# Optimization experiments

Measured on AMD Instinct MI355X. Metric: run time of the kernel, lower is better.

The kernel has to match this reference:

```python
import jax, jax.numpy as jnp
import numpy as np

B, T, D = 4, 4096, 2048
W_SCALE = 0.02


def setup_inputs() -> dict:
    key = jax.random.key(0)
    ks = jax.random.split(key, 10)
    x = jax.random.normal(ks[0], (B, T, D), dtype=jnp.float32)
    Wk = jax.random.normal(ks[1], (D, D), dtype=jnp.float32) * W_SCALE
    Wv = jax.random.normal(ks[2], (D, D), dtype=jnp.float32) * W_SCALE
    Wr = jax.random.normal(ks[3], (D, D), dtype=jnp.float32) * W_SCALE
    Wo = jax.random.normal(ks[4], (D, D), dtype=jnp.float32) * W_SCALE
    bk = jnp.zeros((D,), jnp.float32)
    bv = jnp.zeros((D,), jnp.float32)
    br = jnp.zeros((D,), jnp.float32)
    bo = jnp.zeros((D,), jnp.float32)
    tmk = jax.random.uniform(ks[5], (D,), dtype=jnp.float32)
    tmv = jax.random.uniform(ks[6], (D,), dtype=jnp.float32)
    tmr = jax.random.uniform(ks[7], (D,), dtype=jnp.float32)
    u = jax.random.normal(ks[8], (D,), dtype=jnp.float32) * 0.1
    w = jax.random.uniform(ks[9], (D,), dtype=jnp.float32)  # positive decay
    return {"x": x, "Wk": Wk, "bk": bk, "Wv": Wv, "bv": bv, "Wr": Wr, "br": br,
            "Wo": Wo, "bo": bo, "tmk": tmk, "tmv": tmv, "tmr": tmr, "u": u, "w": w}


def reference(x, Wk, bk, Wv, bv, Wr, br, Wo, bo, tmk, tmv, tmr, u, w):
    # time-shift: xs[:, t] = x[:, t-1], xs[:, 0] = 0  (ZeroPad2d((0,0,1,-1)))
    xs = jnp.pad(x, ((0, 0), (1, 0), (0, 0)))[:, :-1]
    k = x * tmk + xs * (1.0 - tmk)
    v = x * tmv + xs * (1.0 - tmv)
    r = jax.nn.silu(x * tmr + xs * (1.0 - tmr))
    # torch nn.Linear: y = x @ W.T + b
    k = jnp.einsum('btd,ed->bte', k, Wk) + bk
    v = jnp.einsum('btd,ed->bte', v, Wv) + bv
    r = jnp.einsum('btd,ed->bte', r, Wr) + br

    def step(carry, kv_t):
        a, b = carry  # (B, D) each
        k_t, v_t = kv_t
        t = jnp.maximum(u + k_t, w)
        e1 = jnp.exp(-w - t)
        e2 = jnp.exp(u + k_t - t)
        a = e1 * a + e2 * v_t
        b = e1 * b + e2
        return (a, b), a / b

    a0 = jnp.zeros((x.shape[0], x.shape[2]), x.dtype)
    b0 = jnp.zeros_like(a0)
    # scan over time: (T, B, D)
    _, wkv = jax.lax.scan(step, (a0, b0), (k.transpose(1, 0, 2), v.transpose(1, 0, 2)))
    wkv = wkv.transpose(1, 0, 2)  # (B, T, D)
    return jnp.einsum('btd,ed->bte', wkv * r, Wo) + bo
```

## Files before the change

kernel.cpp:

```cpp
#include <hip/hip_runtime.h>
#include <hip/hip_bf16.h>

#define Bb 4
#define Tt 4096
#define Dd 2048
#define Mm (Bb*Tt)
#define CHUNK 64
#define NCHUNK (Tt/CHUNK)

typedef short  short8  __attribute__((ext_vector_type(8)));
typedef float  floatx4 __attribute__((ext_vector_type(4)));

static __device__ __forceinline__ short f2bf(float f) {
    union { float f; unsigned u; } x; x.f = f;
    unsigned r = x.u + 0x7fffu + ((x.u >> 16) & 1u);
    return (short)(r >> 16);
}
static __device__ __forceinline__ float bf2f(short s) {
    union { unsigned u; float f; } x; x.u = ((unsigned)(unsigned short)s) << 16;
    return x.f;
}
static __device__ __forceinline__ float siluf(float v) { return v / (1.f + __expf(-v)); }
static __device__ __forceinline__ float mixf(float xv, float sv, float tv) {
    return fmaf(tv, xv - sv, sv);
}

#define GLDS16(gp, lp) __builtin_amdgcn_global_load_lds( \
    (const __attribute__((address_space(1))) void*)(gp), \
    (__attribute__((address_space(3))) void*)(lp), 16, 0, 0)

static __device__ __forceinline__ short8 pack8(float4 a, float4 b) {
    short8 r;
    r[0]=f2bf(a.x); r[1]=f2bf(a.y); r[2]=f2bf(a.z); r[3]=f2bf(a.w);
    r[4]=f2bf(b.x); r[5]=f2bf(b.y); r[6]=f2bf(b.z); r[7]=f2bf(b.w);
    return r;
}

__global__ __launch_bounds__(256)
void prep_w(const float* __restrict__ w0, const float* __restrict__ w1,
            const float* __restrict__ w2, const float* __restrict__ w3,
            short* __restrict__ o0, short* __restrict__ o1,
            short* __restrict__ o2, short* __restrict__ o3)
{
    const float* s; short* d;
    switch (blockIdx.y) {
        case 0: s = w0; d = o0; break;
        case 1: s = w1; d = o1; break;
        case 2: s = w2; d = o2; break;
        default: s = w3; d = o3; break;
    }
    const size_t e = ((size_t)blockIdx.x * 256 + threadIdx.x) * 8;
    float4 a = *(const float4*)(s + e);
    float4 b = *(const float4*)(s + e + 4);
    *(short8*)(d + e) = pack8(a, b);
}

__global__ __launch_bounds__(256)
void prep_a(const float* __restrict__ x,
            const float* __restrict__ tmk, const float* __restrict__ tmv,
            const float* __restrict__ tmr,
            short* __restrict__ ka, short* __restrict__ va, short* __restrict__ ra)
{
    const size_t e = ((size_t)blockIdx.x * 256 + threadIdx.x) * 8;
    const size_t row = e >> 11;
    const int    col = (int)(e & (Dd - 1));
    const int    t   = (int)(row & (Tt - 1));

    const float* xp = x + e;
    float4 x0 = *(const float4*)xp, x1 = *(const float4*)(xp + 4);
    float4 s0 = make_float4(0,0,0,0), s1 = make_float4(0,0,0,0);
    if (t > 0) { s0 = *(const float4*)(xp - Dd); s1 = *(const float4*)(xp - Dd + 4); }

    float4 tk0 = *(const float4*)(tmk + col), tk1 = *(const float4*)(tmk + col + 4);
    float4 tv0 = *(const float4*)(tmv + col), tv1 = *(const float4*)(tmv + col + 4);
    float4 tr0 = *(const float4*)(tmr + col), tr1 = *(const float4*)(tmr + col + 4);

    float4 k0 = make_float4(mixf(x0.x,s0.x,tk0.x), mixf(x0.y,s0.y,tk0.y),
                            mixf(x0.z,s0.z,tk0.z), mixf(x0.w,s0.w,tk0.w));
    float4 k1 = make_float4(mixf(x1.x,s1.x,tk1.x), mixf(x1.y,s1.y,tk1.y),
                            mixf(x1.z,s1.z,tk1.z), mixf(x1.w,s1.w,tk1.w));
    float4 v0 = make_float4(mixf(x0.x,s0.x,tv0.x), mixf(x0.y,s0.y,tv0.y),
                            mixf(x0.z,s0.z,tv0.z), mixf(x0.w,s0.w,tv0.w));
    float4 v1 = make_float4(mixf(x1.x,s1.x,tv1.x), mixf(x1.y,s1.y,tv1.y),
                            mixf(x1.z,s1.z,tv1.z), mixf(x1.w,s1.w,tv1.w));
    float4 r0 = make_float4(siluf(mixf(x0.x,s0.x,tr0.x)), siluf(mixf(x0.y,s0.y,tr0.y)),
                            siluf(mixf(x0.z,s0.z,tr0.z)), siluf(mixf(x0.w,s0.w,tr0.w)));
    float4 r1 = make_float4(siluf(mixf(x1.x,s1.x,tr1.x)), siluf(mixf(x1.y,s1.y,tr1.y)),
                            siluf(mixf(x1.z,s1.z,tr1.z)), siluf(mixf(x1.w,s1.w,tr1.w)));

    *(short8*)(ka + e) = pack8(k0, k1);
    *(short8*)(va + e) = pack8(v0, v1);
    *(short8*)(ra + e) = pack8(r0, r1);
}

template<int OUTBF>
__global__ __launch_bounds__(256)
void gemm_bf16(const short* __restrict__ A, const short* __restrict__ B,
               const float* __restrict__ bias, void* __restrict__ Cout)
{
    __shared__ short As[128*32];
    __shared__ short Bs[128*32];

    const int tid  = threadIdx.x;
    const int lane = tid & 63, wave = tid >> 6;
    const int row0 = blockIdx.x * 128;
    const int col0 = blockIdx.y * 128;

    const int srow = wave * 32 + (lane >> 2);
    const int scol = (lane & 3) * 8;
    const short* Ag0 = A + (size_t)(row0 + srow) * Dd + scol;
    const short* Ag1 = Ag0 + (size_t)16 * Dd;
    const short* Bg0 = B + (size_t)(col0 + srow) * Dd + scol;
    const short* Bg1 = Bg0 + (size_t)16 * Dd;
    short* Al0 = As + (wave * 32     ) * 32;
    short* Al1 = As + (wave * 32 + 16) * 32;
    short* Bl0 = Bs + (wave * 32     ) * 32;
    short* Bl1 = Bs + (wave * 32 + 16) * 32;

    const int wm = (wave >> 1) * 64, wn = (wave & 1) * 64;
    const int fm = lane & 15, fq = lane >> 4;

    floatx4 acc[4][4];
    #pragma unroll
    for (int i = 0; i < 4; i++)
        #pragma unroll
        for (int j = 0; j < 4; j++) acc[i][j] = (floatx4){0.f,0.f,0.f,0.f};

    for (int k0 = 0; k0 < Dd; k0 += 32) {
        __syncthreads();
        GLDS16(Ag0, Al0);
        GLDS16(Ag1, Al1);
        GLDS16(Bg0, Bl0);
        GLDS16(Bg1, Bl1);
        Ag0 += 32; Ag1 += 32; Bg0 += 32; Bg1 += 32;
        __syncthreads();

        short8 af[4], bfv[4];
        #pragma unroll
        for (int i = 0; i < 4; i++)
            af[i] = *(const short8*)(As + (wm + i*16 + fm)*32 + fq*8);
        #pragma unroll
        for (int j = 0; j < 4; j++)
            bfv[j] = *(const short8*)(Bs + (wn + j*16 + fm)*32 + fq*8);
        #pragma unroll
        for (int i = 0; i < 4; i++)
            #pragma unroll
            for (int j = 0; j < 4; j++)
                acc[i][j] = __builtin_amdgcn_mfma_f32_16x16x32_bf16(af[i], bfv[j], acc[i][j], 0, 0, 0);
    }

    #pragma unroll
    for (int j = 0; j < 4; j++) {
        const int gc = col0 + wn + j*16 + fm;
        const float bj = bias[gc];
        #pragma unroll
        for (int i = 0; i < 4; i++) {
            const int gr = row0 + wm + i*16 + fq*4;
            #pragma unroll
            for (int r = 0; r < 4; r++) {
                const float v = acc[i][j][r] + bj;
                if constexpr (OUTBF)
                    ((short*)Cout)[(size_t)(gr + r) * Dd + gc] = f2bf(v);
                else
                    ((float*)Cout)[(size_t)(gr + r) * Dd + gc] = v;
            }
        }
    }
}

__global__ __launch_bounds__(256)
void scan1(const short* __restrict__ K, const short* __restrict__ V,
           const float* __restrict__ u, const float* __restrict__ w,
           float* __restrict__ Asum, float* __restrict__ Bsum, float* __restrict__ Dsum)
{
    const int c = blockIdx.x, b = blockIdx.y;
    const int d = blockIdx.z * 256 + threadIdx.x;
    const float uu = u[d], ww = w[d];
    const size_t base = ((size_t)(b*Tt + c*CHUNK)) * Dd + d;
    float a = 0.f, bb = 0.f, dd = 1.f;
    #pragma unroll 4
    for (int t = 0; t < CHUNK; t++) {
        const float k = bf2f(K[base + (size_t)t*Dd]);
        const float v = bf2f(V[base + (size_t)t*Dd]);
        const float tt = fmaxf(uu + k, ww);
        const float e1 = __expf(-ww - tt);
        const float e2 = __expf(uu + k - tt);
        a  = e1*a  + e2*v;
        bb = e1*bb + e2;
        dd *= e1;
    }
    const size_t idx = ((size_t)c*Bb + b) * Dd + d;
    Asum[idx] = a; Bsum[idx] = bb; Dsum[idx] = dd;
}

__global__ __launch_bounds__(256)
void scan2(const float* __restrict__ Asum, const float* __restrict__ Bsum,
           const float* __restrict__ Dsum, float* __restrict__ Sa, float* __restrict__ Sb)
{
    const int g = blockIdx.x * 256 + threadIdx.x;
    float a = 0.f, bb = 0.f;
    for (int c = 0; c < NCHUNK; c++) {
        const size_t idx = (size_t)c * (Bb*Dd) + g;
        Sa[idx] = a; Sb[idx] = bb;
        const float dd = Dsum[idx];
        a  = dd*a  + Asum[idx];
        bb = dd*bb + Bsum[idx];
    }
}

__global__ __launch_bounds__(256)
void scan3(const short* __restrict__ K, const short* __restrict__ V,
           const short* __restrict__ R,
           const float* __restrict__ Sa, const float* __restrict__ Sb,
           const float* __restrict__ u, const float* __restrict__ w,
           short* __restrict__ AF)
{
    const int c = blockIdx.x, b = blockIdx.y;
    const int d = blockIdx.z * 256 + threadIdx.x;
    const float uu = u[d], ww = w[d];
    const size_t sidx = ((size_t)c*Bb + b) * Dd + d;
    float a = Sa[sidx], bb = Sb[sidx];
    const size_t base = ((size_t)(b*Tt + c*CHUNK)) * Dd + d;
    #pragma unroll 4
    for (int t = 0; t < CHUNK; t++) {
        const float k = bf2f(K[base + (size_t)t*Dd]);
        const float v = bf2f(V[base + (size_t)t*Dd]);
        const float tt = fmaxf(uu + k, ww);
        const float e1 = __expf(-ww - tt);
        const float e2 = __expf(uu + k - tt);
        a  = e1*a  + e2*v;
        bb = e1*bb + e2;
        const float wkv = a / bb;
        const float r = bf2f(R[base + (size_t)t*Dd]);
        AF[base + (size_t)t*Dd] = f2bf(wkv * r);
    }
}

extern "C" void kernel_launch(void* const* d_in, const int* in_sizes, int n_in,
                              void* d_out, int out_size, void* d_ws, size_t ws_size,
                              hipStream_t stream)
{
    const float* x   = (const float*)d_in[0];
    const float* Wk  = (const float*)d_in[1];
    const float* bk  = (const float*)d_in[2];
    const float* Wv  = (const float*)d_in[3];
    const float* bv  = (const float*)d_in[4];
    const float* Wr  = (const float*)d_in[5];
    const float* br  = (const float*)d_in[6];
    const float* Wo  = (const float*)d_in[7];
    const float* bo  = (const float*)d_in[8];
    const float* tmk = (const float*)d_in[9];
    const float* tmv = (const float*)d_in[10];
    const float* tmr = (const float*)d_in[11];
    const float* u   = (const float*)d_in[12];
    const float* w   = (const float*)d_in[13];

    char* ws = (char*)d_ws;
    short* Wkb  = (short*)(ws + 0x00000000ull);
    short* Wvb  = (short*)(ws + 0x00800000ull);
    short* Wrb  = (short*)(ws + 0x01000000ull);
    short* Wob  = (short*)(ws + 0x01800000ull);
    short* ka   = (short*)(ws + 0x02000000ull);
    short* va   = (short*)(ws + 0x06000000ull);
    short* ra   = (short*)(ws + 0x0A000000ull);
    short* Kb   = (short*)(ws + 0x0E000000ull);
    short* Vb   = (short*)(ws + 0x12000000ull);
    short* Rb   = (short*)(ws + 0x16000000ull);
    float* Asum = (float*)(ws + 0x1A000000ull);
    float* Bsum = (float*)(ws + 0x1A200000ull);
    float* Dsum = (float*)(ws + 0x1A400000ull);
    float* Sa   = (float*)(ws + 0x1A600000ull);
    float* Sb   = (float*)(ws + 0x1A800000ull);
    short* AF   = ka;

    prep_w<<<dim3(2048, 4), 256, 0, stream>>>(Wk, Wv, Wr, Wo, Wkb, Wvb, Wrb, Wob);
    prep_a<<<dim3(16384), 256, 0, stream>>>(x, tmk, tmv, tmr, ka, va, ra);

    dim3 gg(Mm/128, Dd/128);
    gemm_bf16<1><<<gg, 256, 0, stream>>>(ka, Wkb, bk, Kb);
    gemm_bf16<1><<<gg, 256, 0, stream>>>(va, Wvb, bv, Vb);
    gemm_bf16<1><<<gg, 256, 0, stream>>>(ra, Wrb, br, Rb);

    scan1<<<dim3(NCHUNK, Bb, Dd/256), 256, 0, stream>>>(Kb, Vb, u, w, Asum, Bsum, Dsum);
    scan2<<<dim3((Bb*Dd)/256), 256, 0, stream>>>(Asum, Bsum, Dsum, Sa, Sb);
    scan3<<<dim3(NCHUNK, Bb, Dd/256), 256, 0, stream>>>(Kb, Vb, Rb, Sa, Sb, u, w, AF);

    gemm_bf16<0><<<gg, 256, 0, stream>>>(AF, Wob, bo, (float*)d_out);
}
```

Measured before the change: 1.142 ms.

## Use 256x256 pipelined GEMM tiles and vectorize chunked scan kernels

Replaces the 128x128 single-buffered GEMM with a 256x256-tile, 512-thread kernel. The new kernel uses a 4-stage LDS ring with direct global-to-LDS loads, XOR-swizzled LDS addressing, grouped block ordering for L2 reuse, and split barriers with priority bumps around the MFMA bursts. The aim is to cut global traffic per FLOP and hide load latency behind compute. The scan kernels now process 8 channels per thread with 16-byte vector loads and stores, which raises register use and lowers the number of scan blocks.

```diff
diff --git a/kernel.cpp b/kernel.cpp
--- a/kernel.cpp
+++ b/kernel.cpp
@@ -7,6 +7,7 @@
 #define Mm (Bb*Tt)
 #define CHUNK 64
 #define NCHUNK (Tt/CHUNK)
+#define NT (Dd/32)
 
 typedef short  short8  __attribute__((ext_vector_type(8)));
 typedef float  floatx4 __attribute__((ext_vector_type(4)));
@@ -28,6 +29,12 @@
 #define GLDS16(gp, lp) __builtin_amdgcn_global_load_lds( \
     (const __attribute__((address_space(1))) void*)(gp), \
     (__attribute__((address_space(3))) void*)(lp), 16, 0, 0)
+
+#define FENCE() asm volatile("" ::: "memory")
+#define BAR()   do { FENCE(); __builtin_amdgcn_s_barrier(); FENCE(); } while (0)
+#define WAIT_LGKM0() asm volatile("s_waitcnt lgkmcnt(0)" ::: "memory")
+#define WAIT_VM8()   asm volatile("s_waitcnt vmcnt(8)" ::: "memory")
+#define WAIT_VM0()   asm volatile("s_waitcnt vmcnt(0)" ::: "memory")
 
 static __device__ __forceinline__ short8 pack8(float4 a, float4 b) {
     short8 r;
@@ -94,67 +101,132 @@
 }
 
 template<int OUTBF>
-__global__ __launch_bounds__(256)
-void gemm_bf16(const short* __restrict__ A, const short* __restrict__ B,
-               const float* __restrict__ bias, void* __restrict__ Cout)
-{
-    __shared__ short As[128*32];
-    __shared__ short Bs[128*32];
+__global__ __launch_bounds__(512)
+void gemm256(const short* __restrict__ A, const short* __restrict__ B,
+             const float* __restrict__ bias, void* __restrict__ Cout)
+{
+    __shared__ short As[4*8192];
+    __shared__ short Bs[4*8192];
 
     const int tid  = threadIdx.x;
-    const int lane = tid & 63, wave = tid >> 6;
-    const int row0 = blockIdx.x * 128;
-    const int col0 = blockIdx.y * 128;
-
-    const int srow = wave * 32 + (lane >> 2);
-    const int scol = (lane & 3) * 8;
-    const short* Ag0 = A + (size_t)(row0 + srow) * Dd + scol;
-    const short* Ag1 = Ag0 + (size_t)16 * Dd;
-    const short* Bg0 = B + (size_t)(col0 + srow) * Dd + scol;
-    const short* Bg1 = Bg0 + (size_t)16 * Dd;
-    short* Al0 = As + (wave * 32     ) * 32;
-    short* Al1 = As + (wave * 32 + 16) * 32;
-    short* Bl0 = Bs + (wave * 32     ) * 32;
-    short* Bl1 = Bs + (wave * 32 + 16) * 32;
-
-    const int wm = (wave >> 1) * 64, wn = (wave & 1) * 64;
+    const int lane = tid & 63, wv = tid >> 6;
+
+    const int orig = blockIdx.x;
+    const int wg   = (orig & 7) * 64 + (orig >> 3);
+    const int row0 = (wg & 63) * 256;
+    const int col0 = (wg >> 6) * 256;
+
+    const int lofs  = (lane * 16) ^ ((lane >> 3) << 4);
+    const int lrow  = lofs >> 6;
+    const int lcol8 = (lofs >> 4) & 3;
+    const short* Ag = A + (size_t)(row0 + wv * 32 + lrow) * Dd + lcol8 * 8;
+    const short* Bg = B + (size_t)(col0 + wv * 32 + lrow) * Dd + lcol8 * 8;
+    short* Asw = As + wv * 1024;
+    short* Bsw = Bs + wv * 1024;
+
+#define STAGE_A(bufi) do { \
+    GLDS16(Ag,                 Asw + (bufi)*8192); \
+    GLDS16(Ag + (size_t)16*Dd, Asw + (bufi)*8192 + 512); \
+    Ag += 32; } while (0)
+#define STAGE_B(bufi) do { \
+    GLDS16(Bg,                 Bsw + (bufi)*8192); \
+    GLDS16(Bg + (size_t)16*Dd, Bsw + (bufi)*8192 + 512); \
+    Bg += 32; } while (0)
+
     const int fm = lane & 15, fq = lane >> 4;
-
-    floatx4 acc[4][4];
-    #pragma unroll
-    for (int i = 0; i < 4; i++)
+    const int wm = (wv >> 2) * 128;
+    const int wn = (wv & 3) * 64;
+    const int rA = wm + fm, rB = wn + fm;
+    const char* aP = (const char*)As + (((rA * 64) | (fq * 16)) ^ (((rA >> 1) & 7) << 4));
+    const char* bP = (const char*)Bs + (((rB * 64) | (fq * 16)) ^ (((rB >> 1) & 7) << 4));
+
+    floatx4 acc[8][4];
+    #pragma unroll
+    for (int i = 0; i < 8; i++)
         #pragma unroll
         for (int j = 0; j < 4; j++) acc[i][j] = (floatx4){0.f,0.f,0.f,0.f};
 
-    for (int k0 = 0; k0 < Dd; k0 += 32) {
-        __syncthreads();
-        GLDS16(Ag0, Al0);
-        GLDS16(Ag1, Al1);
-        GLDS16(Bg0, Bl0);
-        GLDS16(Bg1, Bl1);
-        Ag0 += 32; Ag1 += 32; Bg0 += 32; Bg1 += 32;
-        __syncthreads();
-
-        short8 af[4], bfv[4];
+    short8 a_[4], b_[4];
+
+    STAGE_A(0); STAGE_B(0);
+    STAGE_A(1); STAGE_B(1);
+    STAGE_A(2); STAGE_B(2);
+    WAIT_VM8();
+    BAR();
+
+    for (int t = 0; t < NT - 3; ++t) {
+        const int bi = t & 3, nb = (t + 3) & 3;
+        #pragma unroll
+        for (int j = 0; j < 4; j++) b_[j] = *(const short8*)(bP + bi * 16384 + j * 1024);
+        #pragma unroll
+        for (int i = 0; i < 4; i++) a_[i] = *(const short8*)(aP + bi * 16384 + i * 1024);
+        STAGE_A(nb);
+        BAR();
+        WAIT_LGKM0(); __builtin_amdgcn_sched_barrier(0);
+        __builtin_amdgcn_s_setprio(1);
         #pragma unroll
         for (int i = 0; i < 4; i++)
-            af[i] = *(const short8*)(As + (wm + i*16 + fm)*32 + fq*8);
-        #pragma unroll
-        for (int j = 0; j < 4; j++)
-            bfv[j] = *(const short8*)(Bs + (wn + j*16 + fm)*32 + fq*8);
+            #pragma unroll
+            for (int j = 0; j < 4; j++)
+                acc[i][j] = __builtin_amdgcn_mfma_f32_16x16x32_bf16(a_[i], b_[j], acc[i][j], 0, 0, 0);
+        __builtin_amdgcn_s_setprio(0);
+        BAR();
+        #pragma unroll
+        for (int i = 0; i < 4; i++) a_[i] = *(const short8*)(aP + bi * 16384 + (4 + i) * 1024);
+        STAGE_B(nb);
+        WAIT_VM8();
+        BAR();
+        WAIT_LGKM0(); __builtin_amdgcn_sched_barrier(0);
+        __builtin_amdgcn_s_setprio(1);
         #pragma unroll
         for (int i = 0; i < 4; i++)
             #pragma unroll
             for (int j = 0; j < 4; j++)
-                acc[i][j] = __builtin_amdgcn_mfma_f32_16x16x32_bf16(af[i], bfv[j], acc[i][j], 0, 0, 0);
-    }
+                acc[4+i][j] = __builtin_amdgcn_mfma_f32_16x16x32_bf16(a_[i], b_[j], acc[4+i][j], 0, 0, 0);
+        __builtin_amdgcn_s_setprio(0);
+        BAR();
+    }
+
+    WAIT_VM0();
+    BAR();
+    for (int t = NT - 3; t < NT; ++t) {
+        const int bi = t & 3;
+        #pragma unroll
+        for (int j = 0; j < 4; j++) b_[j] = *(const short8*)(bP + bi * 16384 + j * 1024);
+        #pragma unroll
+        for (int i = 0; i < 4; i++) a_[i] = *(const short8*)(aP + bi * 16384 + i * 1024);
+        BAR();
+        WAIT_LGKM0(); __builtin_amdgcn_sched_barrier(0);
+        __builtin_amdgcn_s_setprio(1);
+        #pragma unroll
+        for (int i = 0; i < 4; i++)
+            #pragma unroll
+            for (int j = 0; j < 4; j++)
+                acc[i][j] = __builtin_amdgcn_mfma_f32_16x16x32_bf16(a_[i], b_[j], acc[i][j], 0, 0, 0);
+        __builtin_amdgcn_s_setprio(0);
+        BAR();
+        #pragma unroll
+        for (int i = 0; i < 4; i++) a_[i] = *(const short8*)(aP + bi * 16384 + (4 + i) * 1024);
+        BAR();
+        WAIT_LGKM0(); __builtin_amdgcn_sched_barrier(0);
+        __builtin_amdgcn_s_setprio(1);
+        #pragma unroll
+        for (int i = 0; i < 4; i++)
+            #pragma unroll
+            for (int j = 0; j < 4; j++)
+                acc[4+i][j] = __builtin_amdgcn_mfma_f32_16x16x32_bf16(a_[i], b_[j], acc[4+i][j], 0, 0, 0);
+        __builtin_amdgcn_s_setprio(0);
+        BAR();
+    }
+#undef STAGE_A
+#undef STAGE_B
 
     #pragma unroll
     for (int j = 0; j < 4; j++) {
         const int gc = col0 + wn + j*16 + fm;
         const float bj = bias[gc];
         #pragma unroll
-        for (int i = 0; i < 4; i++) {
+        for (int i = 0; i < 8; i++) {
             const int gr = row0 + wm + i*16 + fq*4;
             #pragma unroll
             for (int r = 0; r < 4; r++) {
@@ -174,23 +246,29 @@
            float* __restrict__ Asum, float* __restrict__ Bsum, float* __restrict__ Dsum)
 {
     const int c = blockIdx.x, b = blockIdx.y;
-    const int d = blockIdx.z * 256 + threadIdx.x;
-    const float uu = u[d], ww = w[d];
-    const size_t base = ((size_t)(b*Tt + c*CHUNK)) * Dd + d;
-    float a = 0.f, bb = 0.f, dd = 1.f;
-    #pragma unroll 4
+    const int d0 = threadIdx.x * 8;
+    float uu[8], ww[8], a[8], bb[8], dd[8];
+    #pragma unroll
+    for (int e = 0; e < 8; e++) { uu[e]=u[d0+e]; ww[e]=w[d0+e]; a[e]=0.f; bb[e]=0.f; dd[e]=1.f; }
+    const size_t base = ((size_t)(b*Tt + c*CHUNK)) * Dd + d0;
+    #pragma unroll 2
     for (int t = 0; t < CHUNK; t++) {
-        const float k = bf2f(K[base + (size_t)t*Dd]);
-        const float v = bf2f(V[base + (size_t)t*Dd]);
-        const float tt = fmaxf(uu + k, ww);
-        const float e1 = __expf(-ww - tt);
-        const float e2 = __expf(uu + k - tt);
-        a  = e1*a  + e2*v;
-        bb = e1*bb + e2;
-        dd *= e1;
-    }
-    const size_t idx = ((size_t)c*Bb + b) * Dd + d;
-    Asum[idx] = a; Bsum[idx] = bb; Dsum[idx] = dd;
+        short8 kv = *(const short8*)(K + base + (size_t)t*Dd);
+        short8 vv = *(const short8*)(V + base + (size_t)t*Dd);
+        #pragma unroll
+        for (int e = 0; e < 8; e++) {
+            const float k = bf2f(kv[e]), v = bf2f(vv[e]);
+            const float tt = fmaxf(uu[e] + k, ww[e]);
+            const float e1 = __expf(-ww[e] - tt);
+            const float e2 = __expf(uu[e] + k - tt);
+            a[e]  = e1*a[e]  + e2*v;
+            bb[e] = e1*bb[e] + e2;
+            dd[e] *= e1;
+        }
+    }
+    const size_t idx = ((size_t)c*Bb + b) * Dd + d0;
+    #pragma unroll
+    for (int e = 0; e < 8; e++) { Asum[idx+e]=a[e]; Bsum[idx+e]=bb[e]; Dsum[idx+e]=dd[e]; }
 }
 
 __global__ __launch_bounds__(256)
@@ -216,23 +294,29 @@
            short* __restrict__ AF)
 {
     const int c = blockIdx.x, b = blockIdx.y;
-    const int d = blockIdx.z * 256 + threadIdx.x;
-    const float uu = u[d], ww = w[d];
-    const size_t sidx = ((size_t)c*Bb + b) * Dd + d;
-    float a = Sa[sidx], bb = Sb[sidx];
-    const size_t base = ((size_t)(b*Tt + c*CHUNK)) * Dd + d;
-    #pragma unroll 4
+    const int d0 = threadIdx.x * 8;
+    float uu[8], ww[8], a[8], bb[8];
+    const size_t sidx = ((size_t)c*Bb + b) * Dd + d0;
+    #pragma unroll
+    for (int e = 0; e < 8; e++) { uu[e]=u[d0+e]; ww[e]=w[d0+e]; a[e]=Sa[sidx+e]; bb[e]=Sb[sidx+e]; }
+    const size_t base = ((size_t)(b*Tt + c*CHUNK)) * Dd + d0;
+    #pragma unroll 2
     for (int t = 0; t < CHUNK; t++) {
-        const float k = bf2f(K[base + (size_t)t*Dd]);
-        const float v = bf2f(V[base + (size_t)t*Dd]);
-        const float tt = fmaxf(uu + k, ww);
-        const float e1 = __expf(-ww - tt);
-        const float e2 = __expf(uu + k - tt);
-        a  = e1*a  + e2*v;
-        bb = e1*bb + e2;
-        const float wkv = a / bb;
-        const float r = bf2f(R[base + (size_t)t*Dd]);
-        AF[base + (size_t)t*Dd] = f2bf(wkv * r);
+        short8 kv = *(const short8*)(K + base + (size_t)t*Dd);
+        short8 vv = *(const short8*)(V + base + (size_t)t*Dd);
+        short8 rv = *(const short8*)(R + base + (size_t)t*Dd);
+        short8 ov;
+        #pragma unroll
+        for (int e = 0; e < 8; e++) {
+            const float k = bf2f(kv[e]), v = bf2f(vv[e]);
+            const float tt = fmaxf(uu[e] + k, ww[e]);
+            const float e1 = __expf(-ww[e] - tt);
+            const float e2 = __expf(uu[e] + k - tt);
+            a[e]  = e1*a[e]  + e2*v;
+            bb[e] = e1*bb[e] + e2;
+            ov[e] = f2bf((a[e] / bb[e]) * bf2f(rv[e]));
+        }
+        *(short8*)(AF + base + (size_t)t*Dd) = ov;
     }
 }
 
@@ -276,14 +360,14 @@
     prep_w<<<dim3(2048, 4), 256, 0, stream>>>(Wk, Wv, Wr, Wo, Wkb, Wvb, Wrb, Wob);
     prep_a<<<dim3(16384), 256, 0, stream>>>(x, tmk, tmv, tmr, ka, va, ra);
 
-    dim3 gg(Mm/128, Dd/128);
-    gemm_bf16<1><<<gg, 256, 0, stream>>>(ka, Wkb, bk, Kb);
-    gemm_bf16<1><<<gg, 256, 0, stream>>>(va, Wvb, bv, Vb);
-    gemm_bf16<1><<<gg, 256, 0, stream>>>(ra, Wrb, br, Rb);
-
-    scan1<<<dim3(NCHUNK, Bb, Dd/256), 256, 0, stream>>>(Kb, Vb, u, w, Asum, Bsum, Dsum);
+    dim3 gg((Mm/256) * (Dd/256));
+    gemm256<1><<<gg, 512, 0, stream>>>(ka, Wkb, bk, Kb);
+    gemm256<1><<<gg, 512, 0, stream>>>(va, Wvb, bv, Vb);
+    gemm256<1><<<gg, 512, 0, stream>>>(ra, Wrb, br, Rb);
+
+    scan1<<<dim3(NCHUNK, Bb), 256, 0, stream>>>(Kb, Vb, u, w, Asum, Bsum, Dsum);
     scan2<<<dim3((Bb*Dd)/256), 256, 0, stream>>>(Asum, Bsum, Dsum, Sa, Sb);
-    scan3<<<dim3(NCHUNK, Bb, Dd/256), 256, 0, stream>>>(Kb, Vb, Rb, Sa, Sb, u, w, AF);
-
-    gemm_bf16<0><<<gg, 256, 0, stream>>>(AF, Wob, bo, (float*)d_out);
-}
+    scan3<<<dim3(NCHUNK, Bb), 256, 0, stream>>>(Kb, Vb, Rb, Sa, Sb, u, w, AF);
+
+    gemm256<0><<<gg, 512, 0, stream>>>(AF, Wob, bo, (float*)d_out);
+}
```

New measurement: 1.326 ms. +16.2%, slower.
